# Kernel optimization log

Hardware: AMD Instinct MI355X
Metric: run time of the kernel (lower is better)

## Reference

```python
import jax, jax.numpy as jnp
import numpy as np

B, S, D, H = 4, 2048, 1024, 16
DH = D // H


def setup_inputs() -> dict:
    key = jax.random.key(0)
    ks = jax.random.split(key, 12)
    inv = 1.0 / np.sqrt(D)
    inp = {
        "queries": jax.random.normal(ks[0], (B, S, D), jnp.float32),
        "keys": jax.random.normal(ks[1], (B, S, D), jnp.float32),
        "values": jax.random.normal(ks[2], (B, S, D), jnp.float32),
        # causal mask: 1.0 where attention is disallowed (strictly upper triangle)
        "mask": jnp.triu(jnp.ones((S, S), jnp.float32), k=1)[None, None, :, :],
        "Wq": jax.random.normal(ks[3], (D, D), jnp.float32) * inv,
        "bq": jnp.zeros((D,), jnp.float32),
        "Wk": jax.random.normal(ks[4], (D, D), jnp.float32) * inv,
        "bk": jnp.zeros((D,), jnp.float32),
        "Wv": jax.random.normal(ks[5], (D, D), jnp.float32) * inv,
        "bv": jnp.zeros((D,), jnp.float32),
        "Wo": jax.random.normal(ks[6], (D, D), jnp.float32) * inv,
        "bo": jnp.zeros((D,), jnp.float32),
    }
    return inp


def _split_heads(x):
    # [B, S, D] -> [B, H, S, DH]
    b, s, _ = x.shape
    return x.reshape(b, s, H, DH).transpose(0, 2, 1, 3)


def reference(queries, keys, values, mask, Wq, bq, Wk, bk, Wv, bv, Wo, bo):
    q = _split_heads(queries @ Wq + bq)
    k = _split_heads(keys @ Wk + bk)
    v = _split_heads(values @ Wv + bv)
    scores = jnp.einsum("bhqd,bhkd->bhqk", q, k) / jnp.sqrt(jnp.float32(DH))
    scores = scores + mask * -1e9
    attn = jax.nn.softmax(scores, axis=-1)
    ctx = jnp.einsum("bhqk,bhkd->bhqd", attn, v)  # [B,H,S,DH]
    ctx = ctx.transpose(0, 2, 1, 3).reshape(queries.shape[0], -1, D)
    return ctx @ Wo + bo
```

## Files before the change

kernel.cpp:

```cpp
#include <hip/hip_runtime.h>
#include <hip/hip_bf16.h>

#define S_LEN 2048
#define DMODEL 1024
#define NHEAD 16
#define DHEAD 64
#define BATCH 4
#define MTOT (BATCH * S_LEN)

typedef __attribute__((ext_vector_type(8))) short short8;
typedef __attribute__((ext_vector_type(8))) unsigned short ushort8;
typedef __attribute__((ext_vector_type(4))) unsigned short ushort4v;
typedef __attribute__((ext_vector_type(4))) unsigned int uint4v;
typedef __attribute__((ext_vector_type(4))) float f32x4;

__device__ __forceinline__ unsigned short f2bf(float x) {
    unsigned int u = __float_as_uint(x);
    u += 0x7FFFu + ((u >> 16) & 1u);
    return (unsigned short)(u >> 16);
}

__device__ __forceinline__ unsigned int cvt_pk_bf16(float lo, float hi) {
    unsigned int r;
    asm("v_cvt_pk_bf16_f32 %0, %1, %2" : "=v"(r) : "v"(lo), "v"(hi));
    return r;
}

__global__ __launch_bounds__(256) void k_conv3(const float* __restrict__ s0, const float* __restrict__ s1,
                                               const float* __restrict__ s2,
                                               unsigned short* __restrict__ d0, unsigned short* __restrict__ d1,
                                               unsigned short* __restrict__ d2, int n8) {
    int i = blockIdx.x * 256 + threadIdx.x;
    if (i >= n8) return;
    const float* src = blockIdx.y == 0 ? s0 : (blockIdx.y == 1 ? s1 : s2);
    unsigned short* dst = blockIdx.y == 0 ? d0 : (blockIdx.y == 1 ? d1 : d2);
    const float4* s4 = (const float4*)src;
    float4 a = s4[(size_t)i * 2];
    float4 b = s4[(size_t)i * 2 + 1];
    ushort8 v;
    v[0] = f2bf(a.x); v[1] = f2bf(a.y); v[2] = f2bf(a.z); v[3] = f2bf(a.w);
    v[4] = f2bf(b.x); v[5] = f2bf(b.y); v[6] = f2bf(b.z); v[7] = f2bf(b.w);
    *(ushort8*)(dst + (size_t)i * 8) = v;
}

__global__ __launch_bounds__(256) void k_transpose_w(const float* __restrict__ W0, const float* __restrict__ W1,
                                                     const float* __restrict__ W2, const float* __restrict__ W3,
                                                     unsigned short* __restrict__ T0, unsigned short* __restrict__ T1,
                                                     unsigned short* __restrict__ T2, unsigned short* __restrict__ T3) {
    const float* src; unsigned short* dst;
    switch (blockIdx.z) {
        case 0: src = W0; dst = T0; break;
        case 1: src = W1; dst = T1; break;
        case 2: src = W2; dst = T2; break;
        default: src = W3; dst = T3; break;
    }
    __shared__ float t[32][33];
    int tx = threadIdx.x & 31, ty = threadIdx.x >> 5;
    int n0 = blockIdx.x * 32, k0 = blockIdx.y * 32;
#pragma unroll
    for (int i = 0; i < 32; i += 8)
        t[ty + i][tx] = src[(size_t)(k0 + ty + i) * DMODEL + n0 + tx];
    __syncthreads();
#pragma unroll
    for (int i = 0; i < 32; i += 8)
        dst[(size_t)(n0 + ty + i) * DMODEL + k0 + tx] = f2bf(t[tx][ty + i]);
}

__global__ __launch_bounds__(256) void k_gemm_qkv(const unsigned short* __restrict__ Xq,
                                                  const unsigned short* __restrict__ Xk,
                                                  const unsigned short* __restrict__ Xv,
                                                  const unsigned short* __restrict__ Tq,
                                                  const unsigned short* __restrict__ Tk,
                                                  const unsigned short* __restrict__ Tv,
                                                  const float* __restrict__ bqp, const float* __restrict__ bkp,
                                                  const float* __restrict__ bvp,
                                                  unsigned short* __restrict__ Qp, unsigned short* __restrict__ Kp,
                                                  unsigned short* __restrict__ Vt) {
    int z = blockIdx.z;
    const unsigned short* A = z == 0 ? Xq : (z == 1 ? Xk : Xv);
    const unsigned short* Bt = z == 0 ? Tq : (z == 1 ? Tk : Tv);
    const float* bias = z == 0 ? bqp : (z == 1 ? bkp : bvp);
    float alpha = z == 0 ? 0.125f * 1.4426950408889634f : 1.0f;

    __shared__ unsigned short Al[128 * 32];
    __shared__ unsigned short Bl[128 * 32];
    int tid = threadIdx.x;
    int wid = tid >> 6, lane = tid & 63;
    int lr = lane & 15, lg = lane >> 4;
    int lin = blockIdx.y * 8 + blockIdx.x;
    int tile = (lin & 7) * 64 + (lin >> 3);
    int bm = (tile >> 3) * 128, bn = (tile & 7) * 128;
    int wm = (wid >> 1) * 64, wn = (wid & 1) * 64;

    f32x4 acc[4][4];
#pragma unroll
    for (int mt = 0; mt < 4; ++mt)
#pragma unroll
        for (int nt = 0; nt < 4; ++nt) acc[mt][nt] = (f32x4)0.0f;

    for (int k0 = 0; k0 < DMODEL; k0 += 32) {
#pragma unroll
        for (int i = 0; i < 2; ++i) {
            int c = (wid * 2 + i) * 64 + lane;
            int row = c >> 2, cc = c & 3;
            const unsigned short* ga = A + (size_t)(bm + row) * DMODEL + k0 + cc * 8;
            const unsigned short* gb = Bt + (size_t)(bn + row) * DMODEL + k0 + cc * 8;
            __builtin_amdgcn_global_load_lds((const __attribute__((address_space(1))) unsigned int*)ga,
                                             (__attribute__((address_space(3))) unsigned int*)(Al + (wid * 2 + i) * 512),
                                             16, 0, 0);
            __builtin_amdgcn_global_load_lds((const __attribute__((address_space(1))) unsigned int*)gb,
                                             (__attribute__((address_space(3))) unsigned int*)(Bl + (wid * 2 + i) * 512),
                                             16, 0, 0);
        }
        __syncthreads();
        short8 af[4], bf[4];
#pragma unroll
        for (int mt = 0; mt < 4; ++mt)
            af[mt] = *(const short8*)(Al + (wm + mt * 16 + lr) * 32 + lg * 8);
#pragma unroll
        for (int nt = 0; nt < 4; ++nt)
            bf[nt] = *(const short8*)(Bl + (wn + nt * 16 + lr) * 32 + lg * 8);
        __builtin_amdgcn_s_setprio(1);
#pragma unroll
        for (int mt = 0; mt < 4; ++mt)
#pragma unroll
            for (int nt = 0; nt < 4; ++nt)
                acc[mt][nt] = __builtin_amdgcn_mfma_f32_16x16x32_bf16(af[mt], bf[nt], acc[mt][nt], 0, 0, 0);
        __builtin_amdgcn_s_setprio(0);
        __syncthreads();
    }

#pragma unroll
    for (int nt = 0; nt < 4; ++nt) {
        int col = bn + wn + nt * 16 + lr;
        float bv = bias[col];
#pragma unroll
        for (int mt = 0; mt < 4; ++mt) {
#pragma unroll
            for (int r = 0; r < 4; ++r) {
                int row = bm + wm + mt * 16 + lg * 4 + r;
                float v = (acc[mt][nt][r] + bv) * alpha;
                if (z < 2) {
                    unsigned short* dst = z == 0 ? Qp : Kp;
                    dst[(size_t)row * DMODEL + col] = f2bf(v);
                } else {
                    int h = col >> 6, d = col & 63;
                    int b = row >> 11, s = row & 2047;
                    Vt[((size_t)(b * NHEAD + h) * DHEAD + d) * S_LEN + s] = f2bf(v);
                }
            }
        }
    }
}

__global__ __launch_bounds__(256) void k_gemm_out(const unsigned short* __restrict__ A,
                                                  const unsigned short* __restrict__ Bt,
                                                  const float* __restrict__ bias,
                                                  float* __restrict__ Cout) {
    __shared__ unsigned short Al[128 * 32];
    __shared__ unsigned short Bl[128 * 32];
    int tid = threadIdx.x;
    int wid = tid >> 6, lane = tid & 63;
    int lr = lane & 15, lg = lane >> 4;
    int lin = blockIdx.y * 8 + blockIdx.x;
    int tile = (lin & 7) * 64 + (lin >> 3);
    int bm = (tile >> 3) * 128, bn = (tile & 7) * 128;
    int wm = (wid >> 1) * 64, wn = (wid & 1) * 64;

    f32x4 acc[4][4];
#pragma unroll
    for (int mt = 0; mt < 4; ++mt)
#pragma unroll
        for (int nt = 0; nt < 4; ++nt) acc[mt][nt] = (f32x4)0.0f;

    for (int k0 = 0; k0 < DMODEL; k0 += 32) {
#pragma unroll
        for (int i = 0; i < 2; ++i) {
            int c = (wid * 2 + i) * 64 + lane;
            int row = c >> 2, cc = c & 3;
            const unsigned short* ga = A + (size_t)(bm + row) * DMODEL + k0 + cc * 8;
            const unsigned short* gb = Bt + (size_t)(bn + row) * DMODEL + k0 + cc * 8;
            __builtin_amdgcn_global_load_lds((const __attribute__((address_space(1))) unsigned int*)ga,
                                             (__attribute__((address_space(3))) unsigned int*)(Al + (wid * 2 + i) * 512),
                                             16, 0, 0);
            __builtin_amdgcn_global_load_lds((const __attribute__((address_space(1))) unsigned int*)gb,
                                             (__attribute__((address_space(3))) unsigned int*)(Bl + (wid * 2 + i) * 512),
                                             16, 0, 0);
        }
        __syncthreads();
        short8 af[4], bf[4];
#pragma unroll
        for (int mt = 0; mt < 4; ++mt)
            af[mt] = *(const short8*)(Al + (wm + mt * 16 + lr) * 32 + lg * 8);
#pragma unroll
        for (int nt = 0; nt < 4; ++nt)
            bf[nt] = *(const short8*)(Bl + (wn + nt * 16 + lr) * 32 + lg * 8);
        __builtin_amdgcn_s_setprio(1);
#pragma unroll
        for (int mt = 0; mt < 4; ++mt)
#pragma unroll
            for (int nt = 0; nt < 4; ++nt)
                acc[mt][nt] = __builtin_amdgcn_mfma_f32_16x16x32_bf16(af[mt], bf[nt], acc[mt][nt], 0, 0, 0);
        __builtin_amdgcn_s_setprio(0);
        __syncthreads();
    }

#pragma unroll
    for (int nt = 0; nt < 4; ++nt) {
        int col = bn + wn + nt * 16 + lr;
        float bv = bias[col];
#pragma unroll
        for (int mt = 0; mt < 4; ++mt)
#pragma unroll
            for (int r = 0; r < 4; ++r) {
                int row = bm + wm + mt * 16 + lg * 4 + r;
                Cout[(size_t)row * DMODEL + col] = acc[mt][nt][r] + bv;
            }
    }
}

__global__ __launch_bounds__(128) void k_attn(const unsigned short* __restrict__ Qp,
                                              const unsigned short* __restrict__ Kp,
                                              const unsigned short* __restrict__ Vt,
                                              unsigned short* __restrict__ Ctx) {
    __shared__ f32x4 cbuf[4][4][64];
    __shared__ float mbuf[4][64];
    __shared__ float lbuf[4][64];

    int tid = threadIdx.x;
    int wid = tid >> 6;
    int lane = tid & 63;
    int lr = lane & 15, lg = lane >> 4;
    int bid = blockIdx.x;
    int xcd = bid & 7;
    int j = bid >> 3;
    int bh = xcd + 8 * (j & 7);
    int qb = (S_LEN / 64 - 1) - (j >> 3);
    int b = bh >> 4, h = bh & 15;
    size_t baserow = (size_t)b * S_LEN;
    int hcol = h * DHEAD;

    short8 qf[4][2];
#pragma unroll
    for (int qt = 0; qt < 4; ++qt)
#pragma unroll
        for (int ks = 0; ks < 2; ++ks)
            qf[qt][ks] = *(const short8*)(Qp + (baserow + qb * 64 + qt * 16 + lr) * DMODEL + hcol + ks * 32 + lg * 8);

    f32x4 ctx[4][4];
#pragma unroll
    for (int dt = 0; dt < 4; ++dt)
#pragma unroll
        for (int qt = 0; qt < 4; ++qt) ctx[dt][qt] = (f32x4)0.0f;

    float mrun[4], lrun[4];
#pragma unroll
    for (int qt = 0; qt < 4; ++qt) { mrun[qt] = -1e30f; lrun[qt] = 0.0f; }

    const unsigned short* vth = Vt + (size_t)bh * DHEAD * S_LEN;

    for (int kb = wid; kb <= qb; kb += 2) {
        f32x4 s[4][4];
#pragma unroll
        for (int kt = 0; kt < 4; ++kt)
#pragma unroll
            for (int qt = 0; qt < 4; ++qt) s[kt][qt] = (f32x4)0.0f;
#pragma unroll
        for (int kt = 0; kt < 4; ++kt) {
            short8 kf[2];
#pragma unroll
            for (int ks = 0; ks < 2; ++ks)
                kf[ks] = *(const short8*)(Kp + (baserow + kb * 64 + kt * 16 + lr) * DMODEL + hcol + ks * 32 + lg * 8);
            __builtin_amdgcn_s_setprio(1);
#pragma unroll
            for (int qt = 0; qt < 4; ++qt)
#pragma unroll
                for (int ks = 0; ks < 2; ++ks)
                    s[kt][qt] = __builtin_amdgcn_mfma_f32_16x16x32_bf16(kf[ks], qf[qt][ks], s[kt][qt], 0, 0, 0);
            __builtin_amdgcn_s_setprio(0);
        }

        if (kb == qb) {
#pragma unroll
            for (int kt = 0; kt < 4; ++kt)
#pragma unroll
                for (int qt = 0; qt < 4; ++qt)
#pragma unroll
                    for (int r = 0; r < 4; ++r)
                        if (kt * 16 + lg * 4 + r > qt * 16 + lr) s[kt][qt][r] = -1e30f;
        }

        unsigned int pw[4][2][4];
#pragma unroll
        for (int qt = 0; qt < 4; ++qt) {
            float m0 = fmaxf(fmaxf(s[0][qt][0], s[0][qt][1]), fmaxf(s[0][qt][2], s[0][qt][3]));
            float m1 = fmaxf(fmaxf(s[1][qt][0], s[1][qt][1]), fmaxf(s[1][qt][2], s[1][qt][3]));
            float m2 = fmaxf(fmaxf(s[2][qt][0], s[2][qt][1]), fmaxf(s[2][qt][2], s[2][qt][3]));
            float m3 = fmaxf(fmaxf(s[3][qt][0], s[3][qt][1]), fmaxf(s[3][qt][2], s[3][qt][3]));
            float mx = fmaxf(fmaxf(m0, m1), fmaxf(m2, m3));
            mx = fmaxf(mx, __shfl_xor(mx, 16));
            mx = fmaxf(mx, __shfl_xor(mx, 32));
            unsigned long long grow = __ballot(mx > mrun[qt] + 8.0f);
            if (grow) {
                float mnew = fmaxf(mrun[qt], mx);
                float scale = exp2f(mrun[qt] - mnew);
                mrun[qt] = mnew;
                lrun[qt] *= scale;
#pragma unroll
                for (int dt = 0; dt < 4; ++dt)
#pragma unroll
                    for (int r = 0; r < 4; ++r) ctx[dt][qt][r] *= scale;
            }
            float m = mrun[qt];
#pragma unroll
            for (int kt = 0; kt < 4; ++kt)
#pragma unroll
                for (int r = 0; r < 4; ++r) s[kt][qt][r] = exp2f(s[kt][qt][r] - m);
            float r0 = (s[0][qt][0] + s[0][qt][1]) + (s[0][qt][2] + s[0][qt][3]);
            float r1 = (s[1][qt][0] + s[1][qt][1]) + (s[1][qt][2] + s[1][qt][3]);
            float r2 = (s[2][qt][0] + s[2][qt][1]) + (s[2][qt][2] + s[2][qt][3]);
            float r3 = (s[3][qt][0] + s[3][qt][1]) + (s[3][qt][2] + s[3][qt][3]);
            float rs = (r0 + r1) + (r2 + r3);
            rs += __shfl_xor(rs, 16);
            rs += __shfl_xor(rs, 32);
            lrun[qt] += rs;
#pragma unroll
            for (int ks = 0; ks < 2; ++ks) {
                pw[qt][ks][0] = cvt_pk_bf16(s[2 * ks][qt][0], s[2 * ks][qt][1]);
                pw[qt][ks][1] = cvt_pk_bf16(s[2 * ks][qt][2], s[2 * ks][qt][3]);
                pw[qt][ks][2] = cvt_pk_bf16(s[2 * ks + 1][qt][0], s[2 * ks + 1][qt][1]);
                pw[qt][ks][3] = cvt_pk_bf16(s[2 * ks + 1][qt][2], s[2 * ks + 1][qt][3]);
            }
        }

#pragma unroll
        for (int dt = 0; dt < 4; ++dt) {
            const unsigned short* vrow = vth + (size_t)(dt * 16 + lr) * S_LEN + kb * 64 + 4 * lg;
#pragma unroll
            for (int ks = 0; ks < 2; ++ks) {
                ushort4v lo = *(const ushort4v*)(vrow + 32 * ks);
                ushort4v hi = *(const ushort4v*)(vrow + 32 * ks + 16);
                short8 vf;
                vf[0] = (short)lo[0]; vf[1] = (short)lo[1]; vf[2] = (short)lo[2]; vf[3] = (short)lo[3];
                vf[4] = (short)hi[0]; vf[5] = (short)hi[1]; vf[6] = (short)hi[2]; vf[7] = (short)hi[3];
                __builtin_amdgcn_s_setprio(1);
#pragma unroll
                for (int qt = 0; qt < 4; ++qt) {
                    uint4v w = {pw[qt][ks][0], pw[qt][ks][1], pw[qt][ks][2], pw[qt][ks][3]};
                    ctx[dt][qt] = __builtin_amdgcn_mfma_f32_16x16x32_bf16(vf, __builtin_bit_cast(short8, w),
                                                                          ctx[dt][qt], 0, 0, 0);
                }
                __builtin_amdgcn_s_setprio(0);
            }
        }
    }

    if (wid == 1) {
#pragma unroll
        for (int dt = 0; dt < 4; ++dt)
#pragma unroll
            for (int qt = 0; qt < 4; ++qt) cbuf[dt][qt][lane] = ctx[dt][qt];
#pragma unroll
        for (int qt = 0; qt < 4; ++qt) { mbuf[qt][lane] = mrun[qt]; lbuf[qt][lane] = lrun[qt]; }
    }
    __syncthreads();
    if (wid == 0) {
#pragma unroll
        for (int qt = 0; qt < 4; ++qt) {
            float m1 = mbuf[qt][lane], l1 = lbuf[qt][lane];
            float mM = fmaxf(mrun[qt], m1);
            float s0 = exp2f(mrun[qt] - mM), s1 = exp2f(m1 - mM);
            float linv = 1.0f / (lrun[qt] * s0 + l1 * s1);
            float f0 = s0 * linv, f1 = s1 * linv;
#pragma unroll
            for (int dt = 0; dt < 4; ++dt) {
                f32x4 o1 = cbuf[dt][qt][lane];
                float o0 = ctx[dt][qt][0] * f0 + o1[0] * f1;
                float o1v = ctx[dt][qt][1] * f0 + o1[1] * f1;
                float o2 = ctx[dt][qt][2] * f0 + o1[2] * f1;
                float o3 = ctx[dt][qt][3] * f0 + o1[3] * f1;
                unsigned int lo = (unsigned int)f2bf(o0) | ((unsigned int)f2bf(o1v) << 16);
                unsigned int hi = (unsigned int)f2bf(o2) | ((unsigned int)f2bf(o3) << 16);
                uint2 vv; vv.x = lo; vv.y = hi;
                *(uint2*)(Ctx + (baserow + qb * 64 + qt * 16 + lr) * DMODEL + hcol + dt * 16 + lg * 4) = vv;
            }
        }
    }
}

extern "C" void kernel_launch(void* const* d_in, const int* in_sizes, int n_in,
                              void* d_out, int out_size, void* d_ws, size_t ws_size,
                              hipStream_t stream) {
    const float* q_in = (const float*)d_in[0];
    const float* k_in = (const float*)d_in[1];
    const float* v_in = (const float*)d_in[2];
    const float* Wq = (const float*)d_in[4];
    const float* bq = (const float*)d_in[5];
    const float* Wk = (const float*)d_in[6];
    const float* bk = (const float*)d_in[7];
    const float* Wv = (const float*)d_in[8];
    const float* bv = (const float*)d_in[9];
    const float* Wo = (const float*)d_in[10];
    const float* bo = (const float*)d_in[11];

    char* ws = (char*)d_ws;
    const size_t SZ_ACT = (size_t)MTOT * DMODEL * 2;
    const size_t SZ_W = (size_t)DMODEL * DMODEL * 2;
    unsigned short* Xq = (unsigned short*)(ws);
    unsigned short* Xk = (unsigned short*)(ws + SZ_ACT);
    unsigned short* Xv = (unsigned short*)(ws + 2 * SZ_ACT);
    unsigned short* Tq = (unsigned short*)(ws + 3 * SZ_ACT);
    unsigned short* Tk = (unsigned short*)(ws + 3 * SZ_ACT + SZ_W);
    unsigned short* Tv = (unsigned short*)(ws + 3 * SZ_ACT + 2 * SZ_W);
    unsigned short* To = (unsigned short*)(ws + 3 * SZ_ACT + 3 * SZ_W);
    unsigned short* Qp = (unsigned short*)(ws + 3 * SZ_ACT + 4 * SZ_W);
    unsigned short* Kp = (unsigned short*)(ws + 4 * SZ_ACT + 4 * SZ_W);
    unsigned short* Vt = (unsigned short*)(ws + 5 * SZ_ACT + 4 * SZ_W);
    unsigned short* Cx = (unsigned short*)(ws + 6 * SZ_ACT + 4 * SZ_W);

    int n8 = MTOT * DMODEL / 8;
    k_conv3<<<dim3((n8 + 255) / 256, 3), 256, 0, stream>>>(q_in, k_in, v_in, Xq, Xk, Xv, n8);
    k_transpose_w<<<dim3(32, 32, 4), 256, 0, stream>>>(Wq, Wk, Wv, Wo, Tq, Tk, Tv, To);

    k_gemm_qkv<<<dim3(8, 64, 3), 256, 0, stream>>>(Xq, Xk, Xv, Tq, Tk, Tv, bq, bk, bv, Qp, Kp, Vt);

    k_attn<<<dim3((S_LEN / 64) * BATCH * NHEAD), 128, 0, stream>>>(Qp, Kp, Vt, Cx);

    k_gemm_out<<<dim3(8, 64), 256, 0, stream>>>(Cx, To, bo, (float*)d_out);
}
```

Before: 476.3 us.

## Use one wave per attention block, batch softmax reductions, use raw v_exp

The attention kernel now runs a single 64-lane wave per query block and walks every key block itself. This drops the two-wave key split and the shared-memory merge with its barrier at the end. The softmax is restructured so the max and sum shuffles for all four query tiles are batched together. The lazy rescale guarded by a ballot is replaced with an unconditional rescale, and exp2f is swapped for the raw v_exp_f32 instruction. In exchange, each block has half the parallelism, so per-block latency on the long causal rows grows, and the always-on rescale adds multiplies on every iteration.

```diff
diff --git a/kernel.cpp b/kernel.cpp
--- a/kernel.cpp
+++ b/kernel.cpp
@@ -23,6 +23,12 @@
 __device__ __forceinline__ unsigned int cvt_pk_bf16(float lo, float hi) {
     unsigned int r;
     asm("v_cvt_pk_bf16_f32 %0, %1, %2" : "=v"(r) : "v"(lo), "v"(hi));
+    return r;
+}
+
+__device__ __forceinline__ float fast_exp2(float x) {
+    float r;
+    asm("v_exp_f32 %0, %1" : "=v"(r) : "v"(x));
     return r;
 }
 
@@ -219,17 +225,11 @@
     }
 }
 
-__global__ __launch_bounds__(128) void k_attn(const unsigned short* __restrict__ Qp,
-                                              const unsigned short* __restrict__ Kp,
-                                              const unsigned short* __restrict__ Vt,
-                                              unsigned short* __restrict__ Ctx) {
-    __shared__ f32x4 cbuf[4][4][64];
-    __shared__ float mbuf[4][64];
-    __shared__ float lbuf[4][64];
-
-    int tid = threadIdx.x;
-    int wid = tid >> 6;
-    int lane = tid & 63;
+__global__ __launch_bounds__(64) void k_attn(const unsigned short* __restrict__ Qp,
+                                             const unsigned short* __restrict__ Kp,
+                                             const unsigned short* __restrict__ Vt,
+                                             unsigned short* __restrict__ Ctx) {
+    int lane = threadIdx.x & 63;
     int lr = lane & 15, lg = lane >> 4;
     int bid = blockIdx.x;
     int xcd = bid & 7;
@@ -259,7 +259,7 @@
 
     const unsigned short* vth = Vt + (size_t)bh * DHEAD * S_LEN;
 
-    for (int kb = wid; kb <= qb; kb += 2) {
+    for (int kb = 0; kb <= qb; ++kb) {
         f32x4 s[4][4];
 #pragma unroll
         for (int kt = 0; kt < 4; ++kt)
@@ -290,40 +290,65 @@
                         if (kt * 16 + lg * 4 + r > qt * 16 + lr) s[kt][qt][r] = -1e30f;
         }
 
-        unsigned int pw[4][2][4];
+        float mx[4];
 #pragma unroll
         for (int qt = 0; qt < 4; ++qt) {
-            float m0 = fmaxf(fmaxf(s[0][qt][0], s[0][qt][1]), fmaxf(s[0][qt][2], s[0][qt][3]));
-            float m1 = fmaxf(fmaxf(s[1][qt][0], s[1][qt][1]), fmaxf(s[1][qt][2], s[1][qt][3]));
-            float m2 = fmaxf(fmaxf(s[2][qt][0], s[2][qt][1]), fmaxf(s[2][qt][2], s[2][qt][3]));
-            float m3 = fmaxf(fmaxf(s[3][qt][0], s[3][qt][1]), fmaxf(s[3][qt][2], s[3][qt][3]));
-            float mx = fmaxf(fmaxf(m0, m1), fmaxf(m2, m3));
-            mx = fmaxf(mx, __shfl_xor(mx, 16));
-            mx = fmaxf(mx, __shfl_xor(mx, 32));
-            unsigned long long grow = __ballot(mx > mrun[qt] + 8.0f);
-            if (grow) {
-                float mnew = fmaxf(mrun[qt], mx);
-                float scale = exp2f(mrun[qt] - mnew);
-                mrun[qt] = mnew;
-                lrun[qt] *= scale;
-#pragma unroll
-                for (int dt = 0; dt < 4; ++dt)
-#pragma unroll
-                    for (int r = 0; r < 4; ++r) ctx[dt][qt][r] *= scale;
-            }
-            float m = mrun[qt];
+            float a0 = fmaxf(fmaxf(s[0][qt][0], s[0][qt][1]), fmaxf(s[0][qt][2], s[0][qt][3]));
+            float a1 = fmaxf(fmaxf(s[1][qt][0], s[1][qt][1]), fmaxf(s[1][qt][2], s[1][qt][3]));
+            float a2 = fmaxf(fmaxf(s[2][qt][0], s[2][qt][1]), fmaxf(s[2][qt][2], s[2][qt][3]));
+            float a3 = fmaxf(fmaxf(s[3][qt][0], s[3][qt][1]), fmaxf(s[3][qt][2], s[3][qt][3]));
+            mx[qt] = fmaxf(fmaxf(a0, a1), fmaxf(a2, a3));
+        }
+        float tt[4];
+#pragma unroll
+        for (int qt = 0; qt < 4; ++qt) tt[qt] = __shfl_xor(mx[qt], 16);
+#pragma unroll
+        for (int qt = 0; qt < 4; ++qt) mx[qt] = fmaxf(mx[qt], tt[qt]);
+#pragma unroll
+        for (int qt = 0; qt < 4; ++qt) tt[qt] = __shfl_xor(mx[qt], 32);
+#pragma unroll
+        for (int qt = 0; qt < 4; ++qt) mx[qt] = fmaxf(mx[qt], tt[qt]);
+
+#pragma unroll
+        for (int qt = 0; qt < 4; ++qt) {
+            float mnew = fmaxf(mrun[qt], mx[qt]);
+            float sc = fast_exp2(mrun[qt] - mnew);
+            mrun[qt] = mnew;
+            lrun[qt] *= sc;
+#pragma unroll
+            for (int dt = 0; dt < 4; ++dt)
+#pragma unroll
+                for (int r = 0; r < 4; ++r) ctx[dt][qt][r] *= sc;
+        }
+
+#pragma unroll
+        for (int qt = 0; qt < 4; ++qt)
 #pragma unroll
             for (int kt = 0; kt < 4; ++kt)
 #pragma unroll
-                for (int r = 0; r < 4; ++r) s[kt][qt][r] = exp2f(s[kt][qt][r] - m);
+                for (int r = 0; r < 4; ++r) s[kt][qt][r] = fast_exp2(s[kt][qt][r] - mrun[qt]);
+
+        float rs[4];
+#pragma unroll
+        for (int qt = 0; qt < 4; ++qt) {
             float r0 = (s[0][qt][0] + s[0][qt][1]) + (s[0][qt][2] + s[0][qt][3]);
             float r1 = (s[1][qt][0] + s[1][qt][1]) + (s[1][qt][2] + s[1][qt][3]);
             float r2 = (s[2][qt][0] + s[2][qt][1]) + (s[2][qt][2] + s[2][qt][3]);
             float r3 = (s[3][qt][0] + s[3][qt][1]) + (s[3][qt][2] + s[3][qt][3]);
-            float rs = (r0 + r1) + (r2 + r3);
-            rs += __shfl_xor(rs, 16);
-            rs += __shfl_xor(rs, 32);
-            lrun[qt] += rs;
+            rs[qt] = (r0 + r1) + (r2 + r3);
+        }
+#pragma unroll
+        for (int qt = 0; qt < 4; ++qt) tt[qt] = __shfl_xor(rs[qt], 16);
+#pragma unroll
+        for (int qt = 0; qt < 4; ++qt) rs[qt] += tt[qt];
+#pragma unroll
+        for (int qt = 0; qt < 4; ++qt) tt[qt] = __shfl_xor(rs[qt], 32);
+#pragma unroll
+        for (int qt = 0; qt < 4; ++qt) { rs[qt] += tt[qt]; lrun[qt] += rs[qt]; }
+
+        uint4v pw[4][2];
+#pragma unroll
+        for (int qt = 0; qt < 4; ++qt)
 #pragma unroll
             for (int ks = 0; ks < 2; ++ks) {
                 pw[qt][ks][0] = cvt_pk_bf16(s[2 * ks][qt][0], s[2 * ks][qt][1]);
@@ -331,7 +356,6 @@
                 pw[qt][ks][2] = cvt_pk_bf16(s[2 * ks + 1][qt][0], s[2 * ks + 1][qt][1]);
                 pw[qt][ks][3] = cvt_pk_bf16(s[2 * ks + 1][qt][2], s[2 * ks + 1][qt][3]);
             }
-        }
 
 #pragma unroll
         for (int dt = 0; dt < 4; ++dt) {
@@ -345,45 +369,23 @@
                 vf[4] = (short)hi[0]; vf[5] = (short)hi[1]; vf[6] = (short)hi[2]; vf[7] = (short)hi[3];
                 __builtin_amdgcn_s_setprio(1);
 #pragma unroll
-                for (int qt = 0; qt < 4; ++qt) {
-                    uint4v w = {pw[qt][ks][0], pw[qt][ks][1], pw[qt][ks][2], pw[qt][ks][3]};
-                    ctx[dt][qt] = __builtin_amdgcn_mfma_f32_16x16x32_bf16(vf, __builtin_bit_cast(short8, w),
+                for (int qt = 0; qt < 4; ++qt)
+                    ctx[dt][qt] = __builtin_amdgcn_mfma_f32_16x16x32_bf16(vf, __builtin_bit_cast(short8, pw[qt][ks]),
                                                                           ctx[dt][qt], 0, 0, 0);
-                }
                 __builtin_amdgcn_s_setprio(0);
             }
         }
     }
 
-    if (wid == 1) {
-#pragma unroll
-        for (int dt = 0; dt < 4; ++dt)
-#pragma unroll
-            for (int qt = 0; qt < 4; ++qt) cbuf[dt][qt][lane] = ctx[dt][qt];
-#pragma unroll
-        for (int qt = 0; qt < 4; ++qt) { mbuf[qt][lane] = mrun[qt]; lbuf[qt][lane] = lrun[qt]; }
-    }
-    __syncthreads();
-    if (wid == 0) {
-#pragma unroll
-        for (int qt = 0; qt < 4; ++qt) {
-            float m1 = mbuf[qt][lane], l1 = lbuf[qt][lane];
-            float mM = fmaxf(mrun[qt], m1);
-            float s0 = exp2f(mrun[qt] - mM), s1 = exp2f(m1 - mM);
-            float linv = 1.0f / (lrun[qt] * s0 + l1 * s1);
-            float f0 = s0 * linv, f1 = s1 * linv;
-#pragma unroll
-            for (int dt = 0; dt < 4; ++dt) {
-                f32x4 o1 = cbuf[dt][qt][lane];
-                float o0 = ctx[dt][qt][0] * f0 + o1[0] * f1;
-                float o1v = ctx[dt][qt][1] * f0 + o1[1] * f1;
-                float o2 = ctx[dt][qt][2] * f0 + o1[2] * f1;
-                float o3 = ctx[dt][qt][3] * f0 + o1[3] * f1;
-                unsigned int lo = (unsigned int)f2bf(o0) | ((unsigned int)f2bf(o1v) << 16);
-                unsigned int hi = (unsigned int)f2bf(o2) | ((unsigned int)f2bf(o3) << 16);
-                uint2 vv; vv.x = lo; vv.y = hi;
-                *(uint2*)(Ctx + (baserow + qb * 64 + qt * 16 + lr) * DMODEL + hcol + dt * 16 + lg * 4) = vv;
-            }
+#pragma unroll
+    for (int qt = 0; qt < 4; ++qt) {
+        float inv = 1.0f / lrun[qt];
+#pragma unroll
+        for (int dt = 0; dt < 4; ++dt) {
+            unsigned int lo = (unsigned int)f2bf(ctx[dt][qt][0] * inv) | ((unsigned int)f2bf(ctx[dt][qt][1] * inv) << 16);
+            unsigned int hi = (unsigned int)f2bf(ctx[dt][qt][2] * inv) | ((unsigned int)f2bf(ctx[dt][qt][3] * inv) << 16);
+            uint2 vv; vv.x = lo; vv.y = hi;
+            *(uint2*)(Ctx + (baserow + qb * 64 + qt * 16 + lr) * DMODEL + hcol + dt * 16 + lg * 4) = vv;
         }
     }
 }
@@ -424,7 +426,7 @@
 
     k_gemm_qkv<<<dim3(8, 64, 3), 256, 0, stream>>>(Xq, Xk, Xv, Tq, Tk, Tv, bq, bk, bv, Qp, Kp, Vt);
 
-    k_attn<<<dim3((S_LEN / 64) * BATCH * NHEAD), 128, 0, stream>>>(Qp, Kp, Vt, Cx);
+    k_attn<<<dim3((S_LEN / 64) * BATCH * NHEAD), 64, 0, stream>>>(Qp, Kp, Vt, Cx);
 
     k_gemm_out<<<dim3(8, 64), 256, 0, stream>>>(Cx, To, bo, (float*)d_out);
 }
```

Result: faster. 438.6 us (-7.9%).
